# Kernel tuning notes

Hardware: AMD Instinct MI355X
Metric: run time of the kernel (lower is better)

## Reference

```python
import jax, jax.numpy as jnp
import numpy as np

NUM_HEADS = 16
D_MODEL = 2048
DUPLICATES = 4
DEPTH = D_MODEL // NUM_HEADS  # 128
KV_HEADS = NUM_HEADS // DUPLICATES  # 4


def rope(x):
    # x: (b, s, d); RoPE over first 2*(d//2) dims (d even here), as in source
    b, s, d = x.shape
    dim = d // 2
    inv_freq = (10000.0 ** (-jnp.arange(0, dim, dtype=jnp.float32) / dim)).astype(x.dtype)
    pos = jnp.arange(s, dtype=x.dtype)[None, :, None]  # (1, s, 1)
    freqs = pos * inv_freq  # (1, s, dim)
    cos, sin = jnp.cos(freqs), jnp.sin(freqs)
    x1, x2 = x[..., :dim], x[..., dim:]
    return jnp.concatenate([x1 * cos - x2 * sin, x2 * cos + x1 * sin], axis=-1)


def setup_inputs() -> dict:
    key = jax.random.key(0)
    ks = jax.random.split(key, 6)
    b, s = 2, 2048
    x = jax.random.normal(ks[0], (b, s, D_MODEL), dtype=jnp.float32)
    mask = jnp.ones((b, 1, s, s), dtype=bool)
    std = 0.02
    Wq = jax.random.normal(ks[1], (D_MODEL, D_MODEL), dtype=jnp.float32) * std
    Wk = jax.random.normal(ks[2], (D_MODEL, D_MODEL // DUPLICATES), dtype=jnp.float32) * std
    Wv = jax.random.normal(ks[3], (D_MODEL, D_MODEL // DUPLICATES), dtype=jnp.float32) * std
    Wo = jax.random.normal(ks[4], (D_MODEL, D_MODEL), dtype=jnp.float32) * std
    bo = jnp.zeros((1, 1, D_MODEL), dtype=jnp.float32)
    return {"x": x, "mask": mask, "Wq": Wq, "Wk": Wk, "Wv": Wv, "Wo": Wo, "bo": bo}


def reference(x, mask, Wq, Wk, Wv, Wo, bo):
    b, s, d = x.shape
    # QKV projections; RoPE applied on full projected vectors (as in source)
    q = rope(x @ Wq)          # (b, s, d_model)
    k = rope(x @ Wk)          # (b, s, d_model/dup)
    v = x @ Wv                # (b, s, d_model/dup)
    # split heads
    q = q.reshape(b, s, NUM_HEADS, DEPTH).transpose(0, 2, 1, 3)     # (b, H, s, depth)
    k = k.reshape(b, s, KV_HEADS, DEPTH).transpose(0, 2, 1, 3)      # (b, Hkv, s, depth)
    v = v.reshape(b, s, KV_HEADS, DEPTH).transpose(0, 2, 1, 3)
    # GQA repeat (jnp.repeat on head axis, matching source)
    k = jnp.repeat(k, DUPLICATES, axis=1)                            # (b, H, s, depth)
    v = jnp.repeat(v, DUPLICATES, axis=1)
    # scaled dot-product attention (chunking in source is a pure partition of q; math identical)
    logits = jnp.einsum('bhqd,bhkd->bhqk', q, k) / jnp.sqrt(jnp.asarray(DEPTH, x.dtype))
    logits = jnp.where(mask, logits, jnp.asarray(-1e9, x.dtype))
    attn = jax.nn.softmax(logits, axis=-1)
    out = jnp.einsum('bhqk,bhkd->bhqd', attn, v)                     # (b, H, s, depth)
    out = out.transpose(0, 2, 1, 3).reshape(b, s, d)
    return out @ Wo + bo
```

## Files before the change

kernel.cpp:

```cpp
#include <hip/hip_runtime.h>
#include <hip/hip_bf16.h>
#include <stdint.h>

#define NHEADS 16
#define KVHEADS 4
#define DEPTH 128
#define SEQ 2048
#define DM 2048
#define NQKV 3072
#define SCALE 0.08838834764831845f
#define LOG2E 1.4426950408889634f
#define QSCL (SCALE * LOG2E)

using u16 = unsigned short;
using u32 = unsigned int;
using u64 = unsigned long long;
using bf16x8 = __attribute__((ext_vector_type(8))) __bf16;
using f32x4  = __attribute__((ext_vector_type(4))) float;
using f32x16 = __attribute__((ext_vector_type(16))) float;
using u32x4  = __attribute__((ext_vector_type(4))) u32;

__device__ __forceinline__ u16 bits(float f) {
  return __builtin_bit_cast(u16, (__bf16)f);
}
__device__ __forceinline__ u32 pk2(float a, float b) {
  return (u32)bits(a) | ((u32)bits(b) << 16);
}
__device__ __forceinline__ float ex2(float x) {
#if __has_builtin(__builtin_amdgcn_exp2f)
  return __builtin_amdgcn_exp2f(x);
#else
  return exp2f(x);
#endif
}

__device__ __forceinline__ void gll16(const void* g, void* l) {
  __builtin_amdgcn_global_load_lds((const __attribute__((address_space(1))) void*)g,
                                   (__attribute__((address_space(3))) void*)l, 16, 0, 0);
}


__global__ void k_cvt_x(const float4* __restrict__ x, u16* __restrict__ o, int n4) {
  int i = blockIdx.x * 256 + threadIdx.x;
  if (i >= n4) return;
  float4 v = x[i];
  u64 pk = (u64)bits(v.x) | ((u64)bits(v.y) << 16) | ((u64)bits(v.z) << 32) | ((u64)bits(v.w) << 48);
  reinterpret_cast<u64*>(o)[i] = pk;
}

__global__ void k_prep_wqkv(const float* __restrict__ Wq, const float* __restrict__ Wk,
                            const float* __restrict__ Wv, u16* __restrict__ out) {
  __shared__ float tile[32][33];
  int c0 = blockIdx.x * 32, k0 = blockIdx.y * 32;
  int tx = threadIdx.x, ty = threadIdx.y;
  const float* src;
  int scol, sN;
  if (c0 < 2048) { src = Wq; scol = c0; sN = 2048; }
  else if (c0 < 2560) { src = Wk; scol = c0 - 2048; sN = 512; }
  else { src = Wv; scol = c0 - 2560; sN = 512; }
  for (int i = 0; i < 4; i++)
    tile[ty + i * 8][tx] = src[(size_t)(k0 + ty + i * 8) * sN + scol + tx];
  __syncthreads();
  for (int i = 0; i < 4; i++) {
    int c = c0 + ty + i * 8;
    int N;
    if (c < 2048) {
      N = ((c & 1023) >> 4) * 32 + ((c >= 1024) ? 16 : 0) + (c & 15);
    } else if (c < 2560) {
      int cc = c - 2048;
      N = 2048 + ((cc & 255) >> 4) * 32 + ((cc >= 256) ? 16 : 0) + (cc & 15);
    } else {
      N = c;
    }
    out[(size_t)N * 2048 + k0 + tx] = bits(tile[tx][ty + i * 8]);
  }
}

__global__ void k_transpose_w(const float* __restrict__ in, u16* __restrict__ out, int K, int N) {
  __shared__ float tile[32][33];
  int n0 = blockIdx.x * 32, k0 = blockIdx.y * 32;
  int tx = threadIdx.x, ty = threadIdx.y;
  for (int i = 0; i < 4; i++) tile[ty + i * 8][tx] = in[(size_t)(k0 + ty + i * 8) * N + n0 + tx];
  __syncthreads();
  for (int i = 0; i < 4; i++)
    out[(size_t)(n0 + ty + i * 8) * K + k0 + tx] = bits(tile[tx][ty + i * 8]);
}

__global__ void k_trig(float2* __restrict__ tab) {
  int idx = blockIdx.x * 256 + threadIdx.x;
  int s = idx >> 10, j = idx & 1023;
  float inv = expf((float)j * (-9.210340371976184f / 1024.f));
  float f = (float)s * inv;
  float sv, cv;
  sincosf(f, &sv, &cv);
  tab[idx] = make_float2(cv, sv);
}


#define GBAR __builtin_amdgcn_s_barrier()

#define GSTAGE(GBASE, LHALF, KT, ROWB) do {                                   \
  _Pragma("unroll") for (int i_ = 0; i_ < 2; i_++) {                          \
    int rl_ = (l >> 3) + w * 8 + i_ * 64;                                     \
    int cs_ = (l & 7) ^ ((rl_ & 4) >> 1);                                     \
    gll16((GBASE) + (size_t)((ROWB) + rl_) * K + (KT) * 64 + cs_ * 8,         \
          (char*)(LHALF) + w * 1024 + i_ * 8192);                             \
  }                                                                           \
} while (0)

#define LDA8(DB, MH) do {                                                     \
  const char* pa_ = (const char*)lA[DB][wm];                                  \
  _Pragma("unroll") for (int mi_ = 0; mi_ < 4; mi_++)                         \
  _Pragma("unroll") for (int kk_ = 0; kk_ < 2; kk_++) {                       \
    int row_ = (MH) * 64 + mi_ * 16 + lr;                                     \
    af[mi_ * 2 + kk_] = *(const bf16x8*)(pa_ + row_ * 128 +                   \
        (((kk_ * 4 + lg) ^ ((row_ & 4) >> 1)) * 16));                         \
  }                                                                           \
} while (0)

#define LDB4(DB, NH) do {                                                     \
  const char* pb_ = (const char*)lB[DB][wn >> 1];                             \
  _Pragma("unroll") for (int ni_ = 0; ni_ < 2; ni_++)                         \
  _Pragma("unroll") for (int kk_ = 0; kk_ < 2; kk_++) {                       \
    int row_ = (wn & 1) * 64 + (NH) * 32 + ni_ * 16 + lr;                     \
    bfr[ni_ * 2 + kk_] = *(const bf16x8*)(pb_ + row_ * 128 +                  \
        (((kk_ * 4 + lg) ^ ((row_ & 4) >> 1)) * 16));                         \
  }                                                                           \
} while (0)

#define PHASE_MFMA(MH, NH) do {                                               \
  __builtin_amdgcn_s_setprio(1);                                             \
  _Pragma("unroll") for (int mi_ = 0; mi_ < 4; mi_++)                         \
  _Pragma("unroll") for (int ni_ = 0; ni_ < 2; ni_++)                         \
  _Pragma("unroll") for (int kk_ = 0; kk_ < 2; kk_++)                         \
    acc[MH][NH][mi_][ni_] = __builtin_amdgcn_mfma_f32_16x16x32_bf16(          \
        af[mi_ * 2 + kk_], bfr[ni_ * 2 + kk_], acc[MH][NH][mi_][ni_], 0, 0, 0); \
  __builtin_amdgcn_s_setprio(0);                                             \
} while (0)

template <int MODE>
__global__ __launch_bounds__(512, 2) void k_gemm256(const u16* __restrict__ A,
                                                    const u16* __restrict__ B,
                                                    float* __restrict__ C, int M, int N, int K,
                                                    const float* __restrict__ bias,
                                                    const float2* __restrict__ tab,
                                                    u16* __restrict__ Qh, u16* __restrict__ Kh,
                                                    u16* __restrict__ Vt) {
  __shared__ __align__(16) u16 lA[2][2][128 * 64];
  __shared__ __align__(16) u16 lB[2][2][128 * 64];
  int nt = N >> 8;
  int nwg = gridDim.x;
  int bid = blockIdx.x;
  int swz = (bid & 7) * (nwg >> 3) + (bid >> 3);
  int bm = swz / nt, bn = swz % nt;
  int tid = threadIdx.x;
  int w = tid >> 6, l = tid & 63;
  int lr = l & 15, lg = l >> 4;
  int wm = w >> 2, wn = w & 3;
  const u16* Abase = A + (size_t)(bm * 256) * K;
  const u16* Bbase = B + (size_t)(bn * 256) * K;
  int NT = K >> 6;

  f32x4 acc[2][2][4][2] = {};

  GSTAGE(Abase, lA[0][0], 0, 0);
  GSTAGE(Abase, lA[0][1], 0, 128);
  GSTAGE(Bbase, lB[0][0], 0, 0);
  GSTAGE(Bbase, lB[0][1], 0, 128);
  GSTAGE(Abase, lA[1][0], 1, 0);
  GSTAGE(Abase, lA[1][1], 1, 128);
  asm volatile("s_waitcnt vmcnt(4)" ::: "memory");
  GBAR;

  for (int j = 0; j < (NT >> 1); j++) {
    int kt1 = 2 * j + 1;
    int kt2 = (2 * j + 2) & (NT - 1);
    int kt3 = (2 * j + 3) & (NT - 1);
    bf16x8 af[8];
    bf16x8 bfr[4];
    LDA8(0, 0);
    LDB4(0, 0);
    GSTAGE(Bbase, lB[1][0], kt1, 0);
    GSTAGE(Bbase, lB[1][1], kt1, 128);
    GBAR;
    PHASE_MFMA(0, 0);
    GBAR;
    LDB4(0, 1);
    GBAR;
    PHASE_MFMA(0, 1);
    GBAR;
    LDA8(0, 1);
    GBAR;
    PHASE_MFMA(1, 1);
    GBAR;
    LDB4(0, 0);
    GSTAGE(Abase, lA[0][0], kt2, 0);
    GSTAGE(Abase, lA[0][1], kt2, 128);
    asm volatile("s_waitcnt vmcnt(4)" ::: "memory");
    GBAR;
    PHASE_MFMA(1, 0);
    GBAR;
    LDA8(1, 0);
    LDB4(1, 0);
    GSTAGE(Bbase, lB[0][0], kt2, 0);
    GSTAGE(Bbase, lB[0][1], kt2, 128);
    GBAR;
    PHASE_MFMA(0, 0);
    GBAR;
    LDB4(1, 1);
    GBAR;
    PHASE_MFMA(0, 1);
    GBAR;
    LDA8(1, 1);
    GBAR;
    PHASE_MFMA(1, 1);
    GBAR;
    LDB4(1, 0);
    GSTAGE(Abase, lA[1][0], kt3, 0);
    GSTAGE(Abase, lA[1][1], kt3, 128);
    asm volatile("s_waitcnt vmcnt(4)" ::: "memory");
    GBAR;
    PHASE_MFMA(1, 0);
    GBAR;
  }
  asm volatile("s_waitcnt vmcnt(0)" ::: "memory");

  if constexpr (MODE == 0) {
    int r0 = bm * 256 + wm * 128, c0 = bn * 256 + wn * 64;
#pragma unroll
    for (int mh = 0; mh < 2; mh++)
#pragma unroll
      for (int mi = 0; mi < 4; mi++)
#pragma unroll
        for (int nh = 0; nh < 2; nh++)
#pragma unroll
          for (int ni = 0; ni < 2; ni++) {
            int col = c0 + nh * 32 + ni * 16 + lr;
            float bv = bias ? bias[col] : 0.f;
#pragma unroll
            for (int r = 0; r < 4; r++) {
              int row = r0 + mh * 64 + mi * 16 + lg * 4 + r;
              C[(size_t)row * N + col] = acc[mh][nh][mi][ni][r] + bv;
            }
          }
  } else {
    int c0 = bn * 256 + wn * 64;
#pragma unroll
    for (int mh = 0; mh < 2; mh++)
#pragma unroll
      for (int mi = 0; mi < 4; mi++) {
        int rowb = bm * 256 + wm * 128 + mh * 64 + mi * 16 + lg * 4;
        int b = rowb >> 11, s = rowb & 2047;
#pragma unroll
        for (int nh = 0; nh < 2; nh++) {
          int col = c0 + nh * 32;
          if (col < 2048) {
            int m = ((col >> 5) << 4) + lr;
            int h = m >> 7, d = m & 127;
            size_t o0 = (((size_t)(b * NHEADS + h) * SEQ) + s) * DEPTH + d;
#pragma unroll
            for (int r = 0; r < 4; r++) {
              float2 cs = tab[(size_t)(s + r) * 1024 + m];
              float v0 = acc[mh][nh][mi][0][r], v1 = acc[mh][nh][mi][1][r];
              Qh[o0 + (size_t)r * DEPTH] = bits((v0 * cs.x - v1 * cs.y) * QSCL);
              Qh[o0 + (size_t)8 * SEQ * DEPTH + (size_t)r * DEPTH] =
                  bits((v1 * cs.x + v0 * cs.y) * QSCL);
            }
          } else if (col < 2560) {
            int mk = (((col - 2048) >> 5) << 4) + lr;
            int h = mk >> 7, d = mk & 127;
            size_t o0 = (((size_t)(b * KVHEADS + h) * SEQ) + s) * DEPTH + d;
#pragma unroll
            for (int r = 0; r < 4; r++) {
              float2 cs = tab[(size_t)(s + r) * 1024 + 4 * mk];
              float v0 = acc[mh][nh][mi][0][r], v1 = acc[mh][nh][mi][1][r];
              Kh[o0 + (size_t)r * DEPTH] = bits(v0 * cs.x - v1 * cs.y);
              Kh[o0 + (size_t)2 * SEQ * DEPTH + (size_t)r * DEPTH] =
                  bits(v1 * cs.x + v0 * cs.y);
            }
          } else {
#pragma unroll
            for (int ni = 0; ni < 2; ni++) {
              int c = col + ni * 16 + lr - 2560;
              int kvh = c >> 7, d = c & 127;
              f32x4 v = acc[mh][nh][mi][ni];
              u64 pk = (u64)bits(v[0]) | ((u64)bits(v[1]) << 16) |
                       ((u64)bits(v[2]) << 32) | ((u64)bits(v[3]) << 48);
              *reinterpret_cast<u64*>(
                  &Vt[(((size_t)(b * KVHEADS + kvh) * DEPTH) + d) * SEQ + s]) = pk;
            }
          }
        }
      }
  }
}

__global__ __launch_bounds__(256, 2) void k_attn(const u16* __restrict__ Qh,
                                                 const u16* __restrict__ Kh,
                                                 const u16* __restrict__ Vt,
                                                 u16* __restrict__ Ao) {
  __shared__ u16 lK[2][64 * 128];
  __shared__ u16 lV[2][128 * 64];
  __shared__ float lsc[4][32];

  int bid = blockIdx.x;
  int swz = (bid & 7) * 64 + (bid >> 3);
  int qt = swz & 15;
  int hd = (swz >> 4) & 3, kvh = (swz >> 6) & 3, b = swz >> 8;
  int h = kvh * 4 + hd;

  int tid = threadIdx.x;
  int w = tid >> 6, l = tid & 63;
  int hi = l >> 5;
  int q32 = l & 31;

  const u16* Kb = Kh + ((size_t)b * KVHEADS + kvh) * SEQ * DEPTH;
  const u16* Vb = Vt + ((size_t)b * KVHEADS + kvh) * DEPTH * SEQ;

  const u16* Qp = Qh + (((size_t)(b * NHEADS + h) * SEQ) + qt * 128 + w * 32 + q32) * DEPTH + hi * 8;
  bf16x8 qf[8];
#pragma unroll
  for (int ds = 0; ds < 8; ds++)
    qf[ds] = *reinterpret_cast<const bf16x8*>(Qp + ds * 16);

  f32x16 oacc[4] = {};
  float mrun = -INFINITY, lrun = 0.f;
  bool lo = (l < 32);

  {
#pragma unroll
    for (int i = 0; i < 4; i++) {
      int g = (w * 4 + i) * 64 + l;
      int kv = g >> 4, c = g & 15;
      gll16(Kb + (size_t)kv * DEPTH + ((c ^ (kv & 7)) << 3), (char*)lK[0] + (w * 4 + i) * 1024);
      int d = g >> 3, cv = g & 7;
      gll16(Vb + (size_t)d * SEQ + ((cv ^ (d & 7)) << 3), (char*)lV[0] + (w * 4 + i) * 1024);
    }
  }
  __syncthreads();

  int cur = 0;
  for (int t = 0; t < 32; t++) {
    if (t < 31) {
      int kv0 = (t + 1) * 64;
#pragma unroll
      for (int i = 0; i < 4; i++) {
        int g = (w * 4 + i) * 64 + l;
        int kv = g >> 4, c = g & 15;
        gll16(Kb + (size_t)(kv0 + kv) * DEPTH + ((c ^ (kv & 7)) << 3),
              (char*)lK[cur ^ 1] + (w * 4 + i) * 1024);
        int d = g >> 3, cv = g & 7;
        gll16(Vb + (size_t)d * SEQ + kv0 + ((cv ^ (d & 7)) << 3),
              (char*)lV[cur ^ 1] + (w * 4 + i) * 1024);
      }
    }

    const u16* lk = lK[cur];
    f32x16 sa[2] = {};
    __builtin_amdgcn_s_setprio(1);
#pragma unroll
    for (int ds = 0; ds < 8; ds++) {
#pragma unroll
      for (int a = 0; a < 2; a++) {
        int kv = a * 32 + q32;
        bf16x8 kf = *reinterpret_cast<const bf16x8*>(
            &lk[kv * DEPTH + (((ds * 2 + hi) ^ (kv & 7)) << 3)]);
        sa[a] = __builtin_amdgcn_mfma_f32_32x32x16_bf16(kf, qf[ds], sa[a], 0, 0, 0);
      }
    }
    __builtin_amdgcn_s_setprio(0);

    float pmax = sa[0][0];
#pragma unroll
    for (int r = 1; r < 16; r++) pmax = fmaxf(pmax, sa[0][r]);
#pragma unroll
    for (int r = 0; r < 16; r++) pmax = fmaxf(pmax, sa[1][r]);
    pmax = fmaxf(pmax, __shfl_xor(pmax, 32, 64));
    if (!__all(pmax - mrun <= 11.54f)) {
      float mnew = fmaxf(mrun, pmax);
      float al = ex2(mrun - mnew);
      mrun = mnew;
      lrun *= al;
#pragma unroll
      for (int db = 0; db < 4; db++)
#pragma unroll
        for (int r = 0; r < 16; r++) oacc[db][r] *= al;
    }
    float ps = 0.f;
#pragma unroll
    for (int a = 0; a < 2; a++)
#pragma unroll
      for (int r = 0; r < 16; r++) {
        float p = ex2(sa[a][r] - mrun);
        sa[a][r] = p;
        ps += p;
      }
    ps += __shfl_xor(ps, 32, 64);
    lrun += ps;

    const u16* lv = lV[cur];
#pragma unroll
    for (int a = 0; a < 2; a++) {
#pragma unroll
      for (int js = 0; js < 2; js++) {
        int base = js * 8;
        u32 A0 = pk2(sa[a][base + 0], sa[a][base + 1]);
        u32 A1 = pk2(sa[a][base + 2], sa[a][base + 3]);
        u32 B0 = pk2(sa[a][base + 4], sa[a][base + 5]);
        u32 B1 = pk2(sa[a][base + 6], sa[a][base + 7]);
        asm volatile("v_permlane32_swap_b32 %0, %1" : "+v"(A0), "+v"(B0));
        asm volatile("v_permlane32_swap_b32 %0, %1" : "+v"(A1), "+v"(B1));
        u32x4 tw;
        tw.x = A0;
        tw.y = A1;
        tw.z = B0;
        tw.w = B1;
        bf16x8 pa = __builtin_bit_cast(bf16x8, tw);
        int ks = a * 2 + js;
        __builtin_amdgcn_s_setprio(1);
#pragma unroll
        for (int db = 0; db < 4; db++) {
          int d = db * 32 + q32;
          bf16x8 vf = *reinterpret_cast<const bf16x8*>(
              &lv[d * 64 + (((ks * 2 + hi) ^ (d & 7)) << 3)]);
          oacc[db] = __builtin_amdgcn_mfma_f32_32x32x16_bf16(pa, vf, oacc[db], 0, 0, 0);
        }
        __builtin_amdgcn_s_setprio(0);
      }
    }

    __syncthreads();
    cur ^= 1;
  }

  if (lo) lsc[w][q32] = 1.f / lrun;
  int q0 = qt * 128 + w * 32;
  u16* ob = Ao + (size_t)b * SEQ * DM + (size_t)h * DEPTH;
#pragma unroll
  for (int db = 0; db < 4; db++)
#pragma unroll
    for (int r = 0; r < 16; r++) {
      int row = (r & 3) + 8 * (r >> 2) + 4 * hi;
      ob[(size_t)(q0 + row) * DM + db * 32 + q32] = bits(oacc[db][r] * lsc[w][row]);
    }
}


extern "C" void kernel_launch(void* const* d_in, const int* in_sizes, int n_in,
                              void* d_out, int out_size, void* d_ws, size_t ws_size,
                              hipStream_t stream) {
  const float* x  = (const float*)d_in[0];
  const float* Wq = (const float*)d_in[2];
  const float* Wk = (const float*)d_in[3];
  const float* Wv = (const float*)d_in[4];
  const float* Wo = (const float*)d_in[5];
  const float* bo = (const float*)d_in[6];
  float* out = (float*)d_out;
  char* ws = (char*)d_ws;

  const size_t OFF_XB  = 0;
  const size_t OFF_WT  = 16777216;
  const size_t OFF_WOT = 29360128;
  const size_t OFF_TAB = 37748736;
  const size_t OFF_QH  = 54525952;
  const size_t OFF_KH  = 71303168;
  const size_t OFF_VT  = 75497472;
  const size_t OFF_AO  = 79691776;

  u16*    xb    = (u16*)(ws + OFF_XB);
  u16*    wqkvT = (u16*)(ws + OFF_WT);
  u16*    woT   = (u16*)(ws + OFF_WOT);
  float2* tab   = (float2*)(ws + OFF_TAB);
  u16*    Qhh   = (u16*)(ws + OFF_QH);
  u16*    Khh   = (u16*)(ws + OFF_KH);
  u16*    Vtt   = (u16*)(ws + OFF_VT);
  u16*    Ao    = (u16*)(ws + OFF_AO);

  dim3 tb(32, 8);
  k_cvt_x<<<8192, 256, 0, stream>>>((const float4*)x, xb, 2097152);
  k_prep_wqkv<<<dim3(96, 64), tb, 0, stream>>>(Wq, Wk, Wv, wqkvT);
  k_transpose_w<<<dim3(64, 64), tb, 0, stream>>>(Wo, woT, 2048, 2048);
  k_trig<<<8192, 256, 0, stream>>>(tab);
  k_gemm256<1><<<192, 512, 0, stream>>>(xb, wqkvT, nullptr, 4096, 3072, 2048, nullptr,
                                        tab, Qhh, Khh, Vtt);
  k_attn<<<512, 256, 0, stream>>>(Qhh, Khh, Vtt, Ao);
  k_gemm256<0><<<128, 512, 0, stream>>>(Ao, woT, out, 4096, 2048, 2048, bo,
                                        nullptr, nullptr, nullptr, nullptr);
}
```

Baseline: 371.8 us.

## Merge prep kernels into one launch and pin LDS waits before MFMA phases

Fuses the four preprocessing kernels (x conversion, Wqkv transpose/permute, Wo transpose, RoPE trig table) into a single kernel, with the block index range selecting the task. This removes three launches and the gaps between them. In the GEMM main loop, the barriers that precede each MFMA phase now have scheduling barriers around them and an explicit lgkmcnt(0) wait. This keeps the compiler from moving LDS reads across the barrier, at the cost of possibly less overlap of LDS loads with MFMA work.

```diff
diff --git a/kernel.cpp b/kernel.cpp
--- a/kernel.cpp
+++ b/kernel.cpp
@@ -39,65 +39,69 @@
                                    (__attribute__((address_space(3))) void*)l, 16, 0, 0);
 }
 
-
-__global__ void k_cvt_x(const float4* __restrict__ x, u16* __restrict__ o, int n4) {
-  int i = blockIdx.x * 256 + threadIdx.x;
-  if (i >= n4) return;
-  float4 v = x[i];
-  u64 pk = (u64)bits(v.x) | ((u64)bits(v.y) << 16) | ((u64)bits(v.z) << 32) | ((u64)bits(v.w) << 48);
-  reinterpret_cast<u64*>(o)[i] = pk;
-}
-
-__global__ void k_prep_wqkv(const float* __restrict__ Wq, const float* __restrict__ Wk,
-                            const float* __restrict__ Wv, u16* __restrict__ out) {
+__global__ void k_prep(const float4* __restrict__ x4, u16* __restrict__ xb,
+                       const float* __restrict__ Wq, const float* __restrict__ Wk,
+                       const float* __restrict__ Wv, u16* __restrict__ wqkvT,
+                       const float* __restrict__ Wo, u16* __restrict__ woT,
+                       float2* __restrict__ tab) {
   __shared__ float tile[32][33];
-  int c0 = blockIdx.x * 32, k0 = blockIdx.y * 32;
-  int tx = threadIdx.x, ty = threadIdx.y;
-  const float* src;
-  int scol, sN;
-  if (c0 < 2048) { src = Wq; scol = c0; sN = 2048; }
-  else if (c0 < 2560) { src = Wk; scol = c0 - 2048; sN = 512; }
-  else { src = Wv; scol = c0 - 2560; sN = 512; }
-  for (int i = 0; i < 4; i++)
-    tile[ty + i * 8][tx] = src[(size_t)(k0 + ty + i * 8) * sN + scol + tx];
-  __syncthreads();
-  for (int i = 0; i < 4; i++) {
-    int c = c0 + ty + i * 8;
-    int N;
-    if (c < 2048) {
-      N = ((c & 1023) >> 4) * 32 + ((c >= 1024) ? 16 : 0) + (c & 15);
-    } else if (c < 2560) {
-      int cc = c - 2048;
-      N = 2048 + ((cc & 255) >> 4) * 32 + ((cc >= 256) ? 16 : 0) + (cc & 15);
-    } else {
-      N = c;
-    }
-    out[(size_t)N * 2048 + k0 + tx] = bits(tile[tx][ty + i * 8]);
+  int bid = blockIdx.x;
+  int tid = threadIdx.x;
+  if (bid < 8192) {
+    int i = bid * 256 + tid;
+    float4 v = x4[i];
+    u64 pk = (u64)bits(v.x) | ((u64)bits(v.y) << 16) | ((u64)bits(v.z) << 32) |
+             ((u64)bits(v.w) << 48);
+    reinterpret_cast<u64*>(xb)[i] = pk;
+  } else if (bid < 14336) {
+    int r = bid - 8192;
+    int c0 = (r % 96) * 32, k0 = (r / 96) * 32;
+    int tx = tid & 31, ty = tid >> 5;
+    const float* src;
+    int scol, sN;
+    if (c0 < 2048) { src = Wq; scol = c0; sN = 2048; }
+    else if (c0 < 2560) { src = Wk; scol = c0 - 2048; sN = 512; }
+    else { src = Wv; scol = c0 - 2560; sN = 512; }
+    for (int i = 0; i < 4; i++)
+      tile[ty + i * 8][tx] = src[(size_t)(k0 + ty + i * 8) * sN + scol + tx];
+    __syncthreads();
+    for (int i = 0; i < 4; i++) {
+      int c = c0 + ty + i * 8;
+      int N;
+      if (c < 2048) {
+        N = ((c & 1023) >> 4) * 32 + ((c >= 1024) ? 16 : 0) + (c & 15);
+      } else if (c < 2560) {
+        int cc = c - 2048;
+        N = 2048 + ((cc & 255) >> 4) * 32 + ((cc >= 256) ? 16 : 0) + (cc & 15);
+      } else {
+        N = c;
+      }
+      wqkvT[(size_t)N * 2048 + k0 + tx] = bits(tile[tx][ty + i * 8]);
+    }
+  } else if (bid < 18432) {
+    int r = bid - 14336;
+    int n0 = (r & 63) * 32, k0 = (r >> 6) * 32;
+    int tx = tid & 31, ty = tid >> 5;
+    for (int i = 0; i < 4; i++)
+      tile[ty + i * 8][tx] = Wo[(size_t)(k0 + ty + i * 8) * 2048 + n0 + tx];
+    __syncthreads();
+    for (int i = 0; i < 4; i++)
+      woT[(size_t)(n0 + ty + i * 8) * 2048 + k0 + tx] = bits(tile[tx][ty + i * 8]);
+  } else {
+    int idx = (bid - 18432) * 256 + tid;
+    int s = idx >> 10, j = idx & 1023;
+    float inv = expf((float)j * (-9.210340371976184f / 1024.f));
+    float f = (float)s * inv;
+    float sv, cv;
+    sincosf(f, &sv, &cv);
+    tab[idx] = make_float2(cv, sv);
   }
 }
 
-__global__ void k_transpose_w(const float* __restrict__ in, u16* __restrict__ out, int K, int N) {
-  __shared__ float tile[32][33];
-  int n0 = blockIdx.x * 32, k0 = blockIdx.y * 32;
-  int tx = threadIdx.x, ty = threadIdx.y;
-  for (int i = 0; i < 4; i++) tile[ty + i * 8][tx] = in[(size_t)(k0 + ty + i * 8) * N + n0 + tx];
-  __syncthreads();
-  for (int i = 0; i < 4; i++)
-    out[(size_t)(n0 + ty + i * 8) * K + k0 + tx] = bits(tile[tx][ty + i * 8]);
-}
-
-__global__ void k_trig(float2* __restrict__ tab) {
-  int idx = blockIdx.x * 256 + threadIdx.x;
-  int s = idx >> 10, j = idx & 1023;
-  float inv = expf((float)j * (-9.210340371976184f / 1024.f));
-  float f = (float)s * inv;
-  float sv, cv;
-  sincosf(f, &sv, &cv);
-  tab[idx] = make_float2(cv, sv);
-}
-
 
 #define GBAR __builtin_amdgcn_s_barrier()
+#define SBAR __builtin_amdgcn_sched_barrier(0)
+#define WAITLDS asm volatile("s_waitcnt lgkmcnt(0)" ::: "memory")
 
 #define GSTAGE(GBASE, LHALF, KT, ROWB) do {                                   \
   _Pragma("unroll") for (int i_ = 0; i_ < 2; i_++) {                          \
@@ -137,6 +141,8 @@
         af[mi_ * 2 + kk_], bfr[ni_ * 2 + kk_], acc[MH][NH][mi_][ni_], 0, 0, 0); \
   __builtin_amdgcn_s_setprio(0);                                             \
 } while (0)
+
+#define PH_ENTER do { SBAR; GBAR; WAITLDS; SBAR; } while (0)
 
 template <int MODE>
 __global__ __launch_bounds__(512, 2) void k_gemm256(const u16* __restrict__ A,
@@ -170,6 +176,7 @@
   GSTAGE(Abase, lA[1][0], 1, 0);
   GSTAGE(Abase, lA[1][1], 1, 128);
   asm volatile("s_waitcnt vmcnt(4)" ::: "memory");
+  SBAR;
   GBAR;
 
   for (int j = 0; j < (NT >> 1); j++) {
@@ -182,44 +189,44 @@
     LDB4(0, 0);
     GSTAGE(Bbase, lB[1][0], kt1, 0);
     GSTAGE(Bbase, lB[1][1], kt1, 128);
-    GBAR;
+    PH_ENTER;
     PHASE_MFMA(0, 0);
     GBAR;
     LDB4(0, 1);
-    GBAR;
+    PH_ENTER;
     PHASE_MFMA(0, 1);
     GBAR;
     LDA8(0, 1);
-    GBAR;
+    PH_ENTER;
     PHASE_MFMA(1, 1);
     GBAR;
     LDB4(0, 0);
     GSTAGE(Abase, lA[0][0], kt2, 0);
     GSTAGE(Abase, lA[0][1], kt2, 128);
     asm volatile("s_waitcnt vmcnt(4)" ::: "memory");
-    GBAR;
+    PH_ENTER;
     PHASE_MFMA(1, 0);
     GBAR;
     LDA8(1, 0);
     LDB4(1, 0);
     GSTAGE(Bbase, lB[0][0], kt2, 0);
     GSTAGE(Bbase, lB[0][1], kt2, 128);
-    GBAR;
+    PH_ENTER;
     PHASE_MFMA(0, 0);
     GBAR;
     LDB4(1, 1);
-    GBAR;
+    PH_ENTER;
     PHASE_MFMA(0, 1);
     GBAR;
     LDA8(1, 1);
-    GBAR;
+    PH_ENTER;
     PHASE_MFMA(1, 1);
     GBAR;
     LDB4(1, 0);
     GSTAGE(Abase, lA[1][0], kt3, 0);
     GSTAGE(Abase, lA[1][1], kt3, 128);
     asm volatile("s_waitcnt vmcnt(4)" ::: "memory");
-    GBAR;
+    PH_ENTER;
     PHASE_MFMA(1, 0);
     GBAR;
   }
@@ -476,11 +483,7 @@
   u16*    Vtt   = (u16*)(ws + OFF_VT);
   u16*    Ao    = (u16*)(ws + OFF_AO);
 
-  dim3 tb(32, 8);
-  k_cvt_x<<<8192, 256, 0, stream>>>((const float4*)x, xb, 2097152);
-  k_prep_wqkv<<<dim3(96, 64), tb, 0, stream>>>(Wq, Wk, Wv, wqkvT);
-  k_transpose_w<<<dim3(64, 64), tb, 0, stream>>>(Wo, woT, 2048, 2048);
-  k_trig<<<8192, 256, 0, stream>>>(tab);
+  k_prep<<<26624, 256, 0, stream>>>((const float4*)x, xb, Wq, Wk, Wv, wqkvT, Wo, woT, tab);
   k_gemm256<1><<<192, 512, 0, stream>>>(xb, wqkvT, nullptr, 4096, 3072, 2048, nullptr,
                                         tab, Qhh, Khh, Vtt);
   k_attn<<<512, 256, 0, stream>>>(Qhh, Khh, Vtt, Ao);
```

After: 365.5 us. Within noise of the previous version (-1.7%).
